# Performance work log

Hardware: AMD Instinct MI355X
Metric: run time of the kernel (lower is better)

## Reference

```python
import jax, jax.numpy as jnp
import numpy as np

D_MODEL = 1024
D_STATE = 16
D_CONV = 4
EXPAND = 2
D_INNER = EXPAND * D_MODEL
DT_RANK = (D_MODEL + 15) // 16  # ceil(d_model/16) = 64
BATCH = 2
SEQLEN = 1024


def _causal_conv_silu(x, w, b):
    # x: (B, d_inner, L); w: (d_inner, 1, k) depthwise; causal left padding k-1
    k = w.shape[-1]
    y = jax.lax.conv_general_dilated(
        x, w, window_strides=(1,), padding=[(k - 1, 0)],
        dimension_numbers=("NCH", "OIH", "NCH"), feature_group_count=x.shape[1])
    return jax.nn.silu(y + b[None, :, None])


def _ssm_scan(dA, dBx):
    # h_t = dA_t * h_{t-1} + dBx_t, parallel associative scan over L (axis=2)
    def op(e1, e2):
        a1, b1 = e1
        a2, b2 = e2
        return (a1 * a2, a2 * b1 + b2)
    return jax.lax.associative_scan(op, (dA, dBx), axis=2)[1]


def _mamba_dir(xz, conv_w, conv_b, xproj_w, dtproj_w, dt_bias, A_log, Dp):
    d_inner = xz.shape[1] // 2
    x, z = xz[:, :d_inner], xz[:, d_inner:]
    u = _causal_conv_silu(x, conv_w, conv_b)                  # (B, d, L)
    x_dbl = jnp.einsum('bdl,kd->bkl', u, xproj_w)             # (B, dt_rank+2n, L)
    n = A_log.shape[1]
    r = dtproj_w.shape[1]
    delta = jnp.einsum('dr,brl->bdl', dtproj_w, x_dbl[:, :r])
    Bm = x_dbl[:, r:r + n]                                    # (B, n, L)
    Cm = x_dbl[:, r + n:]                                     # (B, n, L)
    delta = jax.nn.softplus(delta + dt_bias[None, :, None])
    A = -jnp.exp(A_log)                                       # (d, n)
    dA = jnp.exp(jnp.einsum('bdl,dn->bdln', delta, A))
    dBx = jnp.einsum('bdl,bnl,bdl->bdln', delta, Bm, u)
    h = _ssm_scan(dA, dBx)                                    # (B, d, L, n)
    y = jnp.einsum('bdln,bnl->bdl', h, Cm)
    y = y + Dp[None, :, None] * u
    return y * jax.nn.silu(z)


def setup_inputs() -> dict:
    key = jax.random.key(0)
    ks = jax.random.split(key, 16)
    s_in = 1.0 / np.sqrt(D_MODEL)
    s_x = 1.0 / np.sqrt(D_INNER)
    dt_std = DT_RANK ** -0.5

    def dt_bias_init(k):
        dt = jnp.exp(jax.random.uniform(k, (D_INNER,)) * (np.log(0.1) - np.log(0.001)) + np.log(0.001))
        dt = jnp.clip(dt, 1e-4, None)
        return dt + jnp.log(-jnp.expm1(-dt))  # inverse softplus

    A_log = jnp.log(jnp.tile(jnp.arange(1, D_STATE + 1, dtype=jnp.float32)[None, :], (D_INNER, 1)))
    inp = {
        'hidden_states': jax.random.normal(ks[0], (BATCH, SEQLEN, D_MODEL), jnp.float32),
        'in_proj_w': jax.random.normal(ks[1], (2 * D_INNER, D_MODEL), jnp.float32) * s_in,
        'conv_w': jax.random.normal(ks[2], (D_INNER, 1, D_CONV), jnp.float32) * 0.3,
        'conv_bias': jnp.zeros((D_INNER,), jnp.float32),
        'x_proj_w': jax.random.normal(ks[3], (DT_RANK + 2 * D_STATE, D_INNER), jnp.float32) * s_x,
        'dt_proj_w': jax.random.uniform(ks[4], (D_INNER, DT_RANK), jnp.float32, -dt_std, dt_std),
        'dt_proj_bias': dt_bias_init(ks[5]),
        'A_log': A_log,
        'D_skip': jnp.ones((D_INNER,), jnp.float32),
        'convb_w': jax.random.normal(ks[6], (D_INNER, 1, D_CONV), jnp.float32) * 0.3,
        'convb_bias': jnp.zeros((D_INNER,), jnp.float32),
        'x_proj_b_w': jax.random.normal(ks[7], (DT_RANK + 2 * D_STATE, D_INNER), jnp.float32) * s_x,
        'dt_proj_b_w': jax.random.uniform(ks[8], (D_INNER, DT_RANK), jnp.float32, -dt_std, dt_std),
        'dt_proj_b_bias': dt_bias_init(ks[9]),
        'A_b_log': A_log,
        'D_b_skip': jnp.ones((D_INNER,), jnp.float32),
        'out_proj_w': jax.random.normal(ks[10], (D_MODEL, D_INNER), jnp.float32) * s_x,
    }
    return inp


def reference(hidden_states, in_proj_w, conv_w, conv_bias, x_proj_w, dt_proj_w,
              dt_proj_bias, A_log, D_skip, convb_w, convb_bias, x_proj_b_w,
              dt_proj_b_w, dt_proj_b_bias, A_b_log, D_b_skip, out_proj_w):
    # in_proj (no bias): (B, 2*d_inner, L)
    xz = jnp.einsum('ed,bld->bel', in_proj_w, hidden_states)
    out_f = _mamba_dir(xz, conv_w, conv_bias, x_proj_w, dt_proj_w, dt_proj_bias, A_log, D_skip)
    out_b = _mamba_dir(xz[:, :, ::-1], convb_w, convb_bias, x_proj_b_w, dt_proj_b_w,
                       dt_proj_b_bias, A_b_log, D_b_skip)[:, :, ::-1]
    # if_divide_out=False: just sum then out_proj (no bias)
    return jnp.einsum('bdl,od->blo', out_f + out_b, out_proj_w)
```

## Files before the change

kernel.cpp:

```cpp
#include <hip/hip_runtime.h>
#include <math.h>


typedef _Float16 f16x8 __attribute__((ext_vector_type(8)));
typedef _Float16 f16x4 __attribute__((ext_vector_type(4)));
typedef float    f32x4 __attribute__((ext_vector_type(4)));

#define SCH 32
#define SCL 32

__device__ __forceinline__ void gload_lds16(const void* g, void* l) {
    __builtin_amdgcn_global_load_lds(
        (const __attribute__((address_space(1))) void*)g,
        (__attribute__((address_space(3))) void*)l, 16, 0, 0);
}

__device__ __forceinline__ float softplus_f(float x) {
    float e = __builtin_amdgcn_exp2f(-fabsf(x) * 1.44269504f);
    return fmaxf(x, 0.f) + __builtin_amdgcn_logf(1.f + e) * 0.69314718f;
}

template<int CTRL>
__device__ __forceinline__ float dpp_add(float x) {
    int s = __builtin_amdgcn_update_dpp(0, __builtin_bit_cast(int, x),
                                        CTRL, 0xF, 0xF, true);
    return x + __builtin_bit_cast(float, s);
}

template<int WMW, int WNW, int FM, int FN>
__global__ __launch_bounds__(256)
void gemm_nt_f16(const _Float16* __restrict__ A, const _Float16* __restrict__ B,
                 float* __restrict__ C, int K, int ldc, long sA, long sC)
{
    constexpr int BM = WMW * FM * 16, BN = WNW * FN * 16;
    constexpr int ACH = BM / 8, NCH = (BM + BN) / 8;
    __shared__ __align__(16) _Float16 lds[(BM + BN) * 64];
    A += (long)blockIdx.z * sA;
    C += (long)blockIdx.z * sC;
    const int m0 = blockIdx.y * BM, n0 = blockIdx.x * BN;
    const int t = threadIdx.x, wid = t >> 6, lane = t & 63;
    const int wm = wid / WNW, wn = wid % WNW;
    const int srow = lane >> 3;
    const int skk  = ((lane & 7) ^ srow) * 8;

    f32x4 acc[FM][FN];
#pragma unroll
    for (int i = 0; i < FM; ++i)
#pragma unroll
        for (int j = 0; j < FN; ++j) acc[i][j] = (f32x4){0.f, 0.f, 0.f, 0.f};

    for (int k0 = 0; k0 < K; k0 += 64) {
#pragma unroll
        for (int c = wid; c < NCH; c += 4) {
            const _Float16* gp = (c < ACH)
                ? A + (long)(m0 + c * 8 + srow) * K + k0 + skk
                : B + (long)(n0 + (c - ACH) * 8 + srow) * K + k0 + skk;
            gload_lds16(gp, lds + c * 512);
        }
        __syncthreads();
#pragma unroll
        for (int kw = 0; kw < 2; ++kw) {
            f16x8 af[FM], bf[FN];
#pragma unroll
            for (int i = 0; i < FM; ++i) {
                int r = wm * FM * 16 + i * 16 + (lane & 15);
                af[i] = *(const f16x8*)(lds + r * 64 +
                        (((kw * 4 + (lane >> 4)) ^ (r & 7)) * 8));
            }
#pragma unroll
            for (int j = 0; j < FN; ++j) {
                int r = wn * FN * 16 + j * 16 + (lane & 15);
                bf[j] = *(const f16x8*)(lds + BM * 64 + r * 64 +
                        (((kw * 4 + (lane >> 4)) ^ (r & 7)) * 8));
            }
#pragma unroll
            for (int i = 0; i < FM; ++i)
#pragma unroll
                for (int j = 0; j < FN; ++j)
                    acc[i][j] = __builtin_amdgcn_mfma_f32_16x16x32_f16(
                        af[i], bf[j], acc[i][j], 0, 0, 0);
        }
        __syncthreads();
    }
#pragma unroll
    for (int i = 0; i < FM; ++i)
#pragma unroll
        for (int j = 0; j < FN; ++j) {
            int n = n0 + wn * FN * 16 + j * 16 + (lane & 15);
            int m = m0 + wm * FM * 16 + i * 16 + (lane >> 4) * 4;
            *(f32x4*)&C[(long)n * ldc + m] = acc[i][j];
        }
}

#define XP_SK 8
__global__ __launch_bounds__(256)
void xproj_f16_kernel(const float* __restrict__ u, const _Float16* __restrict__ xw16,
                      float* __restrict__ pb)
{
    __shared__ __align__(16) _Float16 Asw[128 * 64];
    __shared__ __align__(16) _Float16 Bsw[96 * 64];
    const int t = threadIdx.x, wid = t >> 6, lane = t & 63;
    const int wm = wid >> 1, wn = wid & 1;
    const int m0 = blockIdx.x * 128;
    const int sk = blockIdx.y, dirb = blockIdx.z;
    const float* ub = u + (long)dirb * 2048 * 1024;
    const _Float16* Bw = xw16 + (long)(dirb >> 1) * 96 * 2048;
    const int srow = lane >> 3;
    const int skk  = ((lane & 7) ^ srow) * 8;
    const int lloc = (t & 31) * 4;
    const int kslt = t >> 5;

    f32x4 acc[4][3];
#pragma unroll
    for (int i = 0; i < 4; ++i)
#pragma unroll
        for (int j = 0; j < 3; ++j) acc[i][j] = (f32x4){0.f, 0.f, 0.f, 0.f};

    for (int ks = 0; ks < 2048 / XP_SK; ks += 64) {
        const int k0 = sk * (2048 / XP_SK) + ks;
#pragma unroll
        for (int c = wid; c < 12; c += 4)
            gload_lds16(Bw + (long)(c * 8 + srow) * 2048 + k0 + skk, Bsw + c * 512);
        float av[8][4];
#pragma unroll
        for (int kk = 0; kk < 8; ++kk) {
            f32x4 v = *(const f32x4*)&ub[(long)(k0 + kslt * 8 + kk) * 1024 + m0 + lloc];
            av[kk][0] = v.x; av[kk][1] = v.y; av[kk][2] = v.z; av[kk][3] = v.w;
        }
#pragma unroll
        for (int q = 0; q < 4; ++q) {
            int l = lloc + q;
            f16x8 h = {(_Float16)av[0][q], (_Float16)av[1][q], (_Float16)av[2][q],
                       (_Float16)av[3][q], (_Float16)av[4][q], (_Float16)av[5][q],
                       (_Float16)av[6][q], (_Float16)av[7][q]};
            *(f16x8*)(Asw + l * 64 + ((kslt ^ (l & 7)) * 8)) = h;
        }
        __syncthreads();
#pragma unroll
        for (int kw = 0; kw < 2; ++kw) {
            f16x8 af[4], bf[3];
#pragma unroll
            for (int i = 0; i < 4; ++i) {
                int r = wm * 64 + i * 16 + (lane & 15);
                af[i] = *(const f16x8*)(Asw + r * 64 +
                        (((kw * 4 + (lane >> 4)) ^ (r & 7)) * 8));
            }
#pragma unroll
            for (int j = 0; j < 3; ++j) {
                int r = wn * 48 + j * 16 + (lane & 15);
                bf[j] = *(const f16x8*)(Bsw + r * 64 +
                        (((kw * 4 + (lane >> 4)) ^ (r & 7)) * 8));
            }
#pragma unroll
            for (int i = 0; i < 4; ++i)
#pragma unroll
                for (int j = 0; j < 3; ++j)
                    acc[i][j] = __builtin_amdgcn_mfma_f32_16x16x32_f16(
                        af[i], bf[j], acc[i][j], 0, 0, 0);
        }
        __syncthreads();
    }
    float* Cp = pb + ((long)sk * 4 + dirb) * 96 * 1024;
#pragma unroll
    for (int i = 0; i < 4; ++i)
#pragma unroll
        for (int j = 0; j < 3; ++j) {
            int n = wn * 48 + j * 16 + (lane & 15);
            int m = m0 + wm * 64 + i * 16 + (lane >> 4) * 4;
            *(f32x4*)&Cp[(long)n * 1024 + m] = acc[i][j];
        }
}

__global__ __launch_bounds__(256)
void xreduce_kernel(const float* __restrict__ pb, float* __restrict__ xdbl)
{
    int f = (blockIdx.x * 256 + threadIdx.x) * 4;
    f32x4 s = (f32x4){0.f, 0.f, 0.f, 0.f};
#pragma unroll
    for (int sk = 0; sk < XP_SK; ++sk)
        s += *(const f32x4*)(pb + (long)sk * 393216 + f);
    *(f32x4*)(xdbl + f) = s;
}

__global__ __launch_bounds__(256)
void dtproj_f16_kernel(const float* __restrict__ xdbl, const _Float16* __restrict__ dw16,
                       const float* __restrict__ bcat, float* __restrict__ delta)
{
    __shared__ __align__(16) _Float16 Asw[128 * 64];
    __shared__ __align__(16) _Float16 Bsw[128 * 64];
    const int t = threadIdx.x, wid = t >> 6, lane = t & 63;
    const int wm = wid >> 1, wn = wid & 1;
    const int n0 = blockIdx.x * 128, m0 = blockIdx.y * 128;
    const int dirb = blockIdx.z, dir = dirb >> 1;
    const float* Xb = xdbl + (long)dirb * 96 * 1024;
    const _Float16* Bw = dw16 + (long)dir * 2048 * 64;
    const int srow = lane >> 3, skk = ((lane & 7) ^ srow) * 8;
    const int lloc = (t & 31) * 4, kslt = t >> 5;

#pragma unroll
    for (int c = wid; c < 16; c += 4)
        gload_lds16(Bw + (long)(n0 + c * 8 + srow) * 64 + skk, Bsw + c * 512);
    float av[8][4];
#pragma unroll
    for (int kk = 0; kk < 8; ++kk) {
        f32x4 v = *(const f32x4*)&Xb[(long)(kslt * 8 + kk) * 1024 + m0 + lloc];
        av[kk][0] = v.x; av[kk][1] = v.y; av[kk][2] = v.z; av[kk][3] = v.w;
    }
#pragma unroll
    for (int q = 0; q < 4; ++q) {
        int l = lloc + q;
        f16x8 h = {(_Float16)av[0][q], (_Float16)av[1][q], (_Float16)av[2][q],
                   (_Float16)av[3][q], (_Float16)av[4][q], (_Float16)av[5][q],
                   (_Float16)av[6][q], (_Float16)av[7][q]};
        *(f16x8*)(Asw + l * 64 + ((kslt ^ (l & 7)) * 8)) = h;
    }
    __syncthreads();

    f32x4 acc[4][4];
#pragma unroll
    for (int i = 0; i < 4; ++i)
#pragma unroll
        for (int j = 0; j < 4; ++j) acc[i][j] = (f32x4){0.f, 0.f, 0.f, 0.f};
#pragma unroll
    for (int kw = 0; kw < 2; ++kw) {
        f16x8 af[4], bf[4];
#pragma unroll
        for (int i = 0; i < 4; ++i) {
            int r = wm * 64 + i * 16 + (lane & 15);
            af[i] = *(const f16x8*)(Asw + r * 64 +
                    (((kw * 4 + (lane >> 4)) ^ (r & 7)) * 8));
        }
#pragma unroll
        for (int j = 0; j < 4; ++j) {
            int r = wn * 64 + j * 16 + (lane & 15);
            bf[j] = *(const f16x8*)(Bsw + r * 64 +
                    (((kw * 4 + (lane >> 4)) ^ (r & 7)) * 8));
        }
#pragma unroll
        for (int i = 0; i < 4; ++i)
#pragma unroll
            for (int j = 0; j < 4; ++j)
                acc[i][j] = __builtin_amdgcn_mfma_f32_16x16x32_f16(
                    af[i], bf[j], acc[i][j], 0, 0, 0);
    }
    float* Dp = delta + (long)dirb * 2048 * 1024;
#pragma unroll
    for (int j = 0; j < 4; ++j) {
        int dd = n0 + wn * 64 + j * 16 + (lane & 15);
        float bm = bcat[dir * 2048 + dd];
#pragma unroll
        for (int i = 0; i < 4; ++i) {
            int m = m0 + wm * 64 + i * 16 + (lane >> 4) * 4;
            f32x4 v = acc[i][j];
            f32x4 o = {softplus_f(v.x + bm), softplus_f(v.y + bm),
                       softplus_f(v.z + bm), softplus_f(v.w + bm)};
            *(f32x4*)&Dp[(long)dd * 1024 + m] = o;
        }
    }
}

__global__ __launch_bounds__(256)
void cvt_f16_kernel(const float* __restrict__ in, _Float16* __restrict__ out, int n)
{
    int i = (blockIdx.x * 256 + threadIdx.x) * 4;
    if (i + 3 < n) {
        float4 v = *(const float4*)(in + i);
        f16x4 h = {(_Float16)v.x, (_Float16)v.y, (_Float16)v.z, (_Float16)v.w};
        *(f16x4*)(out + i) = h;
    }
}

__global__ __launch_bounds__(256)
void concat_weights(const float* __restrict__ xwf, const float* __restrict__ xwb,
                    const float* __restrict__ dwf, const float* __restrict__ dwb,
                    const float* __restrict__ bf,  const float* __restrict__ bb,
                    _Float16* __restrict__ xw16, _Float16* __restrict__ dw16,
                    float* __restrict__ bcat)
{
    int i = blockIdx.x * 256 + threadIdx.x;
    if (i < 196608) { xw16[i] = (_Float16)xwf[i]; xw16[196608 + i] = (_Float16)xwb[i]; }
    if (i < 131072) { dw16[i] = (_Float16)dwf[i]; dw16[131072 + i] = (_Float16)dwb[i]; }
    if (i < 2048)   { bcat[i]  = bf[i];  bcat[2048 + i] = bb[i]; }
}

__global__ __launch_bounds__(256)
void conv_silu_kernel(const float* __restrict__ xz,
                      const float* __restrict__ wf, const float* __restrict__ bf,
                      const float* __restrict__ wb, const float* __restrict__ bbk,
                      float* __restrict__ u)
{
    long idx = (long)blockIdx.x * 256 + threadIdx.x;
    int l = (int)(idx & 1023);
    long r = idx >> 10;
    int d = (int)(r & 2047);
    int b = (int)((r >> 11) & 1);
    int dir = (int)(r >> 12);
    const float* x = xz + ((long)b * 4096 + d) * 1024;
    const float* w = dir ? wb : wf;
    float s = dir ? bbk[d] : bf[d];
    if (dir == 0) {
#pragma unroll
        for (int j = 0; j < 4; ++j) {
            int p = l - 3 + j;
            if (p >= 0) s = fmaf(w[d * 4 + j], x[p], s);
        }
    } else {
#pragma unroll
        for (int j = 0; j < 4; ++j) {
            int src = l - 3 + j;
            if (src >= 0) s = fmaf(w[d * 4 + j], x[1023 - src], s);
        }
    }
    u[idx] = s / (1.f + __builtin_amdgcn_exp2f(-s * 1.44269504f));
}

__global__ __launch_bounds__(256)
void scan_p1_kernel(const float* __restrict__ u, const float* __restrict__ delta,
                    const float* __restrict__ xdbl,
                    const float* __restrict__ Alf, const float* __restrict__ Alb,
                    float* __restrict__ hend, float* __restrict__ aprod)
{
    __shared__ float sD[64][36], sU[64][36], sB[32][20];
    const int t = threadIdx.x, wid = t >> 6, lane = t & 63;
    const int nl = lane & 3;
    const int dloc = wid * 16 + (lane >> 2);
    const int dblk = blockIdx.x, chunk = blockIdx.y, dirb = blockIdx.z;
    const int d = dblk * 64 + dloc, dir = dirb >> 1;
    const int T0 = chunk * SCL;
    f32x4 Av = *(const f32x4*)((dir ? Alb : Alf) + d * 16 + nl * 4);
    float An2[4] = {-expf(Av.x) * 1.44269504f, -expf(Av.y) * 1.44269504f,
                    -expf(Av.z) * 1.44269504f, -expf(Av.w) * 1.44269504f};
    const float* dp = delta + ((long)dirb * 2048 + dblk * 64) * 1024;
    const float* up = u     + ((long)dirb * 2048 + dblk * 64) * 1024;
    const float* Bp = xdbl  + ((long)dirb * 96 + 64) * 1024;

#pragma unroll
    for (int rep = 0; rep < 2; ++rep) {
        int ii = rep * 256 + t;
        int dd = ii >> 3, q = ii & 7;
        *(f32x4*)&sD[dd][q * 4] = *(const f32x4*)&dp[(long)dd * 1024 + T0 + q * 4];
        *(f32x4*)&sU[dd][q * 4] = *(const f32x4*)&up[(long)dd * 1024 + T0 + q * 4];
    }
#pragma unroll
    for (int rep = 0; rep < 2; ++rep) {
        int ii = rep * 256 + t;
        int n = ii >> 5, tt = ii & 31;
        sB[tt][n] = Bp[(long)n * 1024 + T0 + tt];
    }
    __syncthreads();

    float h[4] = {0.f, 0.f, 0.f, 0.f};
    float S = 0.f;
#pragma unroll 4
    for (int g = 0; g < 8; ++g) {
        f32x4 dlv = *(const f32x4*)&sD[dloc][g * 4];
        f32x4 uuv = *(const f32x4*)&sU[dloc][g * 4];
        float dls[4] = {dlv.x, dlv.y, dlv.z, dlv.w};
        float uus[4] = {uuv.x, uuv.y, uuv.z, uuv.w};
#pragma unroll
        for (int r4 = 0; r4 < 4; ++r4) {
            f32x4 Bv = *(const f32x4*)&sB[g * 4 + r4][nl * 4];
            float Bs[4] = {Bv.x, Bv.y, Bv.z, Bv.w};
            float dl = dls[r4], t1 = dl * uus[r4];
            S += dl;
#pragma unroll
            for (int r = 0; r < 4; ++r)
                h[r] = fmaf(__builtin_amdgcn_exp2f(dl * An2[r]), h[r], t1 * Bs[r]);
        }
    }
    long cb = (((long)dirb * SCH + chunk) * 2048 + d) * 16 + nl * 4;
    *(f32x4*)&hend[cb]  = (f32x4){h[0], h[1], h[2], h[3]};
    *(f32x4*)&aprod[cb] = (f32x4){__builtin_amdgcn_exp2f(S * An2[0]),
                                  __builtin_amdgcn_exp2f(S * An2[1]),
                                  __builtin_amdgcn_exp2f(S * An2[2]),
                                  __builtin_amdgcn_exp2f(S * An2[3])};
}

__global__ __launch_bounds__(256)
void scan_carry_kernel(const float* __restrict__ hend, const float* __restrict__ aprod,
                       float* __restrict__ hinit)
{
    int f = blockIdx.x * 256 + threadIdx.x;
    int dn = f & 32767;
    int dirb = f >> 15;
    long src = (long)dirb * SCH * 32768 + dn;
    long dst = (long)(dirb >> 1) * 4194304 + (long)(dirb & 1) * 1048576 + dn;
    float hcur = 0.f;
#pragma unroll
    for (int c = 0; c < SCH; ++c) {
        hinit[dst + (long)c * 32768] = hcur;
        hcur = hend[src + (long)c * 32768]
             + aprod[src + (long)c * 32768] * hcur;
    }
}

__global__ __launch_bounds__(256)
void scan_p3_kernel(const float* __restrict__ u, const float* __restrict__ delta,
                    const float* __restrict__ xdbl,
                    const float* __restrict__ Alf, const float* __restrict__ Alb,
                    const float* __restrict__ Df, const float* __restrict__ Db,
                    const float* __restrict__ hinit, float* __restrict__ y)
{
    __shared__ float sD[64][36], sU[64][36], sB[32][20], sC[32][20];
    const int t = threadIdx.x, wid = t >> 6, lane = t & 63;
    const int nl = lane & 3;
    const int dloc = wid * 16 + (lane >> 2);
    const int dblk = blockIdx.x, chunk = blockIdx.y, dirb = blockIdx.z;
    const int d = dblk * 64 + dloc, dir = dirb >> 1;
    const int T0 = chunk * SCL;
    f32x4 Av = *(const f32x4*)((dir ? Alb : Alf) + d * 16 + nl * 4);
    float An2[4] = {-expf(Av.x) * 1.44269504f, -expf(Av.y) * 1.44269504f,
                    -expf(Av.z) * 1.44269504f, -expf(Av.w) * 1.44269504f};
    const float Dd = (dir ? Db : Df)[d];
    const float* dp = delta + ((long)dirb * 2048 + dblk * 64) * 1024;
    const float* up = u     + ((long)dirb * 2048 + dblk * 64) * 1024;
    const float* Bp = xdbl  + ((long)dirb * 96 + 64) * 1024;
    const float* Cp = xdbl  + ((long)dirb * 96 + 80) * 1024;
    float* yrow = y + ((long)dirb * 2048 + d) * 1024;

#pragma unroll
    for (int rep = 0; rep < 2; ++rep) {
        int ii = rep * 256 + t;
        int dd = ii >> 3, q = ii & 7;
        *(f32x4*)&sD[dd][q * 4] = *(const f32x4*)&dp[(long)dd * 1024 + T0 + q * 4];
        *(f32x4*)&sU[dd][q * 4] = *(const f32x4*)&up[(long)dd * 1024 + T0 + q * 4];
    }
#pragma unroll
    for (int rep = 0; rep < 2; ++rep) {
        int ii = rep * 256 + t;
        int n = ii >> 5, tt = ii & 31;
        sB[tt][n] = Bp[(long)n * 1024 + T0 + tt];
        sC[tt][n] = Cp[(long)n * 1024 + T0 + tt];
    }
    long cb = (long)(dirb >> 1) * 4194304 + (long)(dirb & 1) * 1048576
            + (long)chunk * 32768 + (long)d * 16 + nl * 4;
    f32x4 h0v = *(const f32x4*)&hinit[cb];
    float h[4] = {h0v.x, h0v.y, h0v.z, h0v.w};
    const bool m[4] = {nl == 0, nl == 1, nl == 2, nl == 3};
    __syncthreads();

#pragma unroll 4
    for (int g = 0; g < 8; ++g) {
        f32x4 dlv = *(const f32x4*)&sD[dloc][g * 4];
        f32x4 uuv = *(const f32x4*)&sU[dloc][g * 4];
        float dls[4] = {dlv.x, dlv.y, dlv.z, dlv.w};
        float uus[4] = {uuv.x, uuv.y, uuv.z, uuv.w};
        float keep = 0.f;
#pragma unroll
        for (int r4 = 0; r4 < 4; ++r4) {
            f32x4 Bv = *(const f32x4*)&sB[g * 4 + r4][nl * 4];
            f32x4 Cv = *(const f32x4*)&sC[g * 4 + r4][nl * 4];
            float Bs[4] = {Bv.x, Bv.y, Bv.z, Bv.w};
            float Cs[4] = {Cv.x, Cv.y, Cv.z, Cv.w};
            float dl = dls[r4], uu = uus[r4];
            float t1 = dl * uu;
#pragma unroll
            for (int r = 0; r < 4; ++r)
                h[r] = fmaf(__builtin_amdgcn_exp2f(dl * An2[r]), h[r], t1 * Bs[r]);
            float p = h[0] * Cs[0];
            p = fmaf(h[1], Cs[1], p);
            p = fmaf(h[2], Cs[2], p);
            p = fmaf(h[3], Cs[3], p);
            p = dpp_add<0xB1>(p);
            p = dpp_add<0x4E>(p);
            float fy = fmaf(Dd, uu, p);
            keep = m[r4] ? fy : keep;
        }
        yrow[T0 + g * 4 + nl] = keep;
    }
}

__global__ __launch_bounds__(256)
void combine_T_kernel(const float* __restrict__ xz, const float* __restrict__ y,
                      _Float16* __restrict__ GT)
{
    __shared__ float Ls[64][65];
    const int d0 = blockIdx.x * 64, l0 = blockIdx.y * 64, b = blockIdx.z;
    const int t = threadIdx.x;
#pragma unroll
    for (int rep = 0; rep < 4; ++rep) {
        int i = rep * 256 + t;
        int dl = i >> 4;
        int lq = (i & 15) * 4;
        const float* zp  = xz + ((long)b * 4096 + 2048 + d0 + dl) * 1024 + l0 + lq;
        const float* yfp = y  + ((long)(b)     * 2048 + d0 + dl) * 1024 + l0 + lq;
        const float* ybp = y  + ((long)(2 + b) * 2048 + d0 + dl) * 1024 + (1020 - l0 - lq);
        float4 vz = *(const float4*)zp;
        float4 vf = *(const float4*)yfp;
        float4 vb = *(const float4*)ybp;
        float zz[4]  = {vz.x, vz.y, vz.z, vz.w};
        float ff[4]  = {vf.x, vf.y, vf.z, vf.w};
        float bbv[4] = {vb.w, vb.z, vb.y, vb.x};
#pragma unroll
        for (int qq = 0; qq < 4; ++qq) {
            float z = zz[qq];
            float sz = z / (1.f + __builtin_amdgcn_exp2f(-z * 1.44269504f));
            Ls[dl][lq + qq] = sz * (ff[qq] + bbv[qq]);
        }
    }
    __syncthreads();
#pragma unroll
    for (int rep = 0; rep < 4; ++rep) {
        int i = rep * 256 + t;
        int ll = i >> 4;
        int dq = (i & 15) * 4;
        f16x4 h = {(_Float16)Ls[dq][ll], (_Float16)Ls[dq + 1][ll],
                   (_Float16)Ls[dq + 2][ll], (_Float16)Ls[dq + 3][ll]};
        *(f16x4*)(GT + ((long)(b * 1024 + l0 + ll)) * 2048 + d0 + dq) = h;
    }
}

extern "C" void kernel_launch(void* const* d_in, const int* in_sizes, int n_in,
                              void* d_out, int out_size, void* d_ws, size_t ws_size,
                              hipStream_t stream)
{
    const float* hidden   = (const float*)d_in[0];
    const float* inproj_w = (const float*)d_in[1];
    const float* conv_w   = (const float*)d_in[2];
    const float* conv_b   = (const float*)d_in[3];
    const float* xproj_w  = (const float*)d_in[4];
    const float* dtproj_w = (const float*)d_in[5];
    const float* dt_bias  = (const float*)d_in[6];
    const float* A_log    = (const float*)d_in[7];
    const float* D_skip   = (const float*)d_in[8];
    const float* convb_w  = (const float*)d_in[9];
    const float* convb_b  = (const float*)d_in[10];
    const float* xprojb_w = (const float*)d_in[11];
    const float* dtprojb_w= (const float*)d_in[12];
    const float* dtb_bias = (const float*)d_in[13];
    const float* Ab_log   = (const float*)d_in[14];
    const float* Db_skip  = (const float*)d_in[15];
    const float* outproj_w= (const float*)d_in[16];
    float* out = (float*)d_out;

    float* ws    = (float*)d_ws;
    float* xz    = ws;
    float* u     = ws + 8388608;
    float* xdbl  = ws + 16777216;
    float* delta = ws + 17170432;
    float* y     = ws + 25559040;
    _Float16* H16    = (_Float16*)u;
    _Float16* Win16  = (_Float16*)(u + 1048576);
    float*    xpb    = delta;
    _Float16* GT     = (_Float16*)delta;
    _Float16* Wout16 = (_Float16*)y;
    _Float16* dw16   = (_Float16*)y;
    float*    bcat   = y + 131072;
    _Float16* xw16   = (_Float16*)(y + 135168);
    float* hend  = y;
    float* aprod = y + 4194304;
    float* hinit = xz;

    hipLaunchKernelGGL(cvt_f16_kernel, dim3(2048), dim3(256), 0, stream,
        hidden, H16, 2097152);
    hipLaunchKernelGGL(cvt_f16_kernel, dim3(4096), dim3(256), 0, stream,
        inproj_w, Win16, 4194304);

    hipLaunchKernelGGL(concat_weights, dim3(768), dim3(256), 0, stream,
        xproj_w, xprojb_w, dtproj_w, dtprojb_w, dt_bias, dtb_bias,
        xw16, dw16, bcat);

    hipLaunchKernelGGL((gemm_nt_f16<2, 2, 4, 4>),
        dim3(32, 8, 2), dim3(256), 0, stream,
        H16, Win16, xz, 1024, 1024, 1048576L, 4194304L);

    hipLaunchKernelGGL(conv_silu_kernel, dim3(32768), dim3(256), 0, stream,
        xz, conv_w, conv_b, convb_w, convb_b, u);

    hipLaunchKernelGGL(xproj_f16_kernel, dim3(8, XP_SK, 4), dim3(256), 0, stream,
        u, xw16, xpb);
    hipLaunchKernelGGL(xreduce_kernel, dim3(384), dim3(256), 0, stream,
        xpb, xdbl);

    hipLaunchKernelGGL(dtproj_f16_kernel, dim3(16, 8, 4), dim3(256), 0, stream,
        xdbl, dw16, bcat, delta);

    hipLaunchKernelGGL(scan_p1_kernel, dim3(32, SCH, 4), dim3(256), 0, stream,
        u, delta, xdbl, A_log, Ab_log, hend, aprod);
    hipLaunchKernelGGL(scan_carry_kernel, dim3(512), dim3(256), 0, stream,
        hend, aprod, hinit);
    hipLaunchKernelGGL(scan_p3_kernel, dim3(32, SCH, 4), dim3(256), 0, stream,
        u, delta, xdbl, A_log, Ab_log, D_skip, Db_skip, hinit, y);

    hipLaunchKernelGGL(combine_T_kernel, dim3(32, 16, 2), dim3(256), 0, stream,
        xz, y, GT);

    hipLaunchKernelGGL(cvt_f16_kernel, dim3(2048), dim3(256), 0, stream,
        outproj_w, Wout16, 2097152);

    hipLaunchKernelGGL((gemm_nt_f16<4, 1, 2, 4>),
        dim3(32, 8, 1), dim3(256), 0, stream,
        Wout16, GT, out, 2048, 1024, 0L, 0L);
}
```

Measured before the change: 199.8 us.

## Store u, delta and y intermediates in fp16 and merge setup conversions

The conv/silu output u, the softplus delta and the scan output y are now kept as fp16 instead of fp32, halving the traffic of the memory-bound scan passes, the x-projection and the combine kernel. The separate weight and input conversion launches, including the out-proj weight conversion, are folded into one setup kernel. Workspace offsets are rearranged to fit the new fp16 buffers. Precision drops for delta and u in the recurrence, which may raise numerical error.

```diff
diff --git a/kernel.cpp b/kernel.cpp
--- a/kernel.cpp
+++ b/kernel.cpp
@@ -94,7 +94,7 @@
 
 #define XP_SK 8
 __global__ __launch_bounds__(256)
-void xproj_f16_kernel(const float* __restrict__ u, const _Float16* __restrict__ xw16,
+void xproj_f16_kernel(const _Float16* __restrict__ u16, const _Float16* __restrict__ xw16,
                       float* __restrict__ pb)
 {
     __shared__ __align__(16) _Float16 Asw[128 * 64];
@@ -103,7 +103,7 @@
     const int wm = wid >> 1, wn = wid & 1;
     const int m0 = blockIdx.x * 128;
     const int sk = blockIdx.y, dirb = blockIdx.z;
-    const float* ub = u + (long)dirb * 2048 * 1024;
+    const _Float16* ub = u16 + (long)dirb * 2048 * 1024;
     const _Float16* Bw = xw16 + (long)(dirb >> 1) * 96 * 2048;
     const int srow = lane >> 3;
     const int skk  = ((lane & 7) ^ srow) * 8;
@@ -121,18 +121,17 @@
 #pragma unroll
         for (int c = wid; c < 12; c += 4)
             gload_lds16(Bw + (long)(c * 8 + srow) * 2048 + k0 + skk, Bsw + c * 512);
-        float av[8][4];
+        _Float16 av[8][4];
 #pragma unroll
         for (int kk = 0; kk < 8; ++kk) {
-            f32x4 v = *(const f32x4*)&ub[(long)(k0 + kslt * 8 + kk) * 1024 + m0 + lloc];
-            av[kk][0] = v.x; av[kk][1] = v.y; av[kk][2] = v.z; av[kk][3] = v.w;
+            f16x4 v = *(const f16x4*)&ub[(long)(k0 + kslt * 8 + kk) * 1024 + m0 + lloc];
+            av[kk][0] = v[0]; av[kk][1] = v[1]; av[kk][2] = v[2]; av[kk][3] = v[3];
         }
 #pragma unroll
         for (int q = 0; q < 4; ++q) {
             int l = lloc + q;
-            f16x8 h = {(_Float16)av[0][q], (_Float16)av[1][q], (_Float16)av[2][q],
-                       (_Float16)av[3][q], (_Float16)av[4][q], (_Float16)av[5][q],
-                       (_Float16)av[6][q], (_Float16)av[7][q]};
+            f16x8 h = {av[0][q], av[1][q], av[2][q], av[3][q],
+                       av[4][q], av[5][q], av[6][q], av[7][q]};
             *(f16x8*)(Asw + l * 64 + ((kslt ^ (l & 7)) * 8)) = h;
         }
         __syncthreads();
@@ -184,7 +183,7 @@
 
 __global__ __launch_bounds__(256)
 void dtproj_f16_kernel(const float* __restrict__ xdbl, const _Float16* __restrict__ dw16,
-                       const float* __restrict__ bcat, float* __restrict__ delta)
+                       const float* __restrict__ bcat, _Float16* __restrict__ delta16)
 {
     __shared__ __align__(16) _Float16 Asw[128 * 64];
     __shared__ __align__(16) _Float16 Bsw[128 * 64];
@@ -243,7 +242,7 @@
                 acc[i][j] = __builtin_amdgcn_mfma_f32_16x16x32_f16(
                     af[i], bf[j], acc[i][j], 0, 0, 0);
     }
-    float* Dp = delta + (long)dirb * 2048 * 1024;
+    _Float16* Dp = delta16 + (long)dirb * 2048 * 1024;
 #pragma unroll
     for (int j = 0; j < 4; ++j) {
         int dd = n0 + wn * 64 + j * 16 + (lane & 15);
@@ -252,42 +251,53 @@
         for (int i = 0; i < 4; ++i) {
             int m = m0 + wm * 64 + i * 16 + (lane >> 4) * 4;
             f32x4 v = acc[i][j];
-            f32x4 o = {softplus_f(v.x + bm), softplus_f(v.y + bm),
-                       softplus_f(v.z + bm), softplus_f(v.w + bm)};
-            *(f32x4*)&Dp[(long)dd * 1024 + m] = o;
-        }
-    }
-}
-
-__global__ __launch_bounds__(256)
-void cvt_f16_kernel(const float* __restrict__ in, _Float16* __restrict__ out, int n)
-{
-    int i = (blockIdx.x * 256 + threadIdx.x) * 4;
-    if (i + 3 < n) {
-        float4 v = *(const float4*)(in + i);
-        f16x4 h = {(_Float16)v.x, (_Float16)v.y, (_Float16)v.z, (_Float16)v.w};
-        *(f16x4*)(out + i) = h;
-    }
-}
-
-__global__ __launch_bounds__(256)
-void concat_weights(const float* __restrict__ xwf, const float* __restrict__ xwb,
-                    const float* __restrict__ dwf, const float* __restrict__ dwb,
-                    const float* __restrict__ bf,  const float* __restrict__ bb,
-                    _Float16* __restrict__ xw16, _Float16* __restrict__ dw16,
-                    float* __restrict__ bcat)
-{
-    int i = blockIdx.x * 256 + threadIdx.x;
-    if (i < 196608) { xw16[i] = (_Float16)xwf[i]; xw16[196608 + i] = (_Float16)xwb[i]; }
-    if (i < 131072) { dw16[i] = (_Float16)dwf[i]; dw16[131072 + i] = (_Float16)dwb[i]; }
-    if (i < 2048)   { bcat[i]  = bf[i];  bcat[2048 + i] = bb[i]; }
+            f16x4 o = {(_Float16)softplus_f(v.x + bm), (_Float16)softplus_f(v.y + bm),
+                       (_Float16)softplus_f(v.z + bm), (_Float16)softplus_f(v.w + bm)};
+            *(f16x4*)&Dp[(long)dd * 1024 + m] = o;
+        }
+    }
+}
+
+__global__ __launch_bounds__(256)
+void setup_kernel(const float* __restrict__ hidden, const float* __restrict__ winp,
+                  const float* __restrict__ woutp,
+                  const float* __restrict__ xwf, const float* __restrict__ xwb,
+                  const float* __restrict__ dwf, const float* __restrict__ dwb,
+                  const float* __restrict__ bf,  const float* __restrict__ bb,
+                  _Float16* __restrict__ H16, _Float16* __restrict__ Win16,
+                  _Float16* __restrict__ Wout16,
+                  _Float16* __restrict__ xw16, _Float16* __restrict__ dw16,
+                  float* __restrict__ bcat)
+{
+    long i4 = ((long)blockIdx.x * 256 + threadIdx.x) * 4;
+    auto cvt4 = [](const float* s) -> f16x4 {
+        float4 v = *(const float4*)s;
+        return (f16x4){(_Float16)v.x, (_Float16)v.y, (_Float16)v.z, (_Float16)v.w};
+    };
+    if (i4 < 4194304) *(f16x4*)(Win16 + i4) = cvt4(winp + i4);
+    if (i4 < 2097152) {
+        *(f16x4*)(H16 + i4)   = cvt4(hidden + i4);
+        *(f16x4*)(Wout16 + i4) = cvt4(woutp + i4);
+    }
+    if (i4 < 196608) {
+        *(f16x4*)(xw16 + i4)          = cvt4(xwf + i4);
+        *(f16x4*)(xw16 + 196608 + i4) = cvt4(xwb + i4);
+    }
+    if (i4 < 131072) {
+        *(f16x4*)(dw16 + i4)          = cvt4(dwf + i4);
+        *(f16x4*)(dw16 + 131072 + i4) = cvt4(dwb + i4);
+    }
+    if (i4 < 2048) {
+        *(float4*)(bcat + i4)        = *(const float4*)(bf + i4);
+        *(float4*)(bcat + 2048 + i4) = *(const float4*)(bb + i4);
+    }
 }
 
 __global__ __launch_bounds__(256)
 void conv_silu_kernel(const float* __restrict__ xz,
                       const float* __restrict__ wf, const float* __restrict__ bf,
                       const float* __restrict__ wb, const float* __restrict__ bbk,
-                      float* __restrict__ u)
+                      _Float16* __restrict__ u16)
 {
     long idx = (long)blockIdx.x * 256 + threadIdx.x;
     int l = (int)(idx & 1023);
@@ -311,16 +321,17 @@
             if (src >= 0) s = fmaf(w[d * 4 + j], x[1023 - src], s);
         }
     }
-    u[idx] = s / (1.f + __builtin_amdgcn_exp2f(-s * 1.44269504f));
-}
-
-__global__ __launch_bounds__(256)
-void scan_p1_kernel(const float* __restrict__ u, const float* __restrict__ delta,
+    u16[idx] = (_Float16)(s / (1.f + __builtin_amdgcn_exp2f(-s * 1.44269504f)));
+}
+
+__global__ __launch_bounds__(256)
+void scan_p1_kernel(const _Float16* __restrict__ u16, const _Float16* __restrict__ delta16,
                     const float* __restrict__ xdbl,
                     const float* __restrict__ Alf, const float* __restrict__ Alb,
                     float* __restrict__ hend, float* __restrict__ aprod)
 {
-    __shared__ float sD[64][36], sU[64][36], sB[32][20];
+    __shared__ _Float16 sD[64][40], sU[64][40];
+    __shared__ float sB[32][20];
     const int t = threadIdx.x, wid = t >> 6, lane = t & 63;
     const int nl = lane & 3;
     const int dloc = wid * 16 + (lane >> 2);
@@ -330,16 +341,14 @@
     f32x4 Av = *(const f32x4*)((dir ? Alb : Alf) + d * 16 + nl * 4);
     float An2[4] = {-expf(Av.x) * 1.44269504f, -expf(Av.y) * 1.44269504f,
                     -expf(Av.z) * 1.44269504f, -expf(Av.w) * 1.44269504f};
-    const float* dp = delta + ((long)dirb * 2048 + dblk * 64) * 1024;
-    const float* up = u     + ((long)dirb * 2048 + dblk * 64) * 1024;
-    const float* Bp = xdbl  + ((long)dirb * 96 + 64) * 1024;
-
-#pragma unroll
-    for (int rep = 0; rep < 2; ++rep) {
-        int ii = rep * 256 + t;
-        int dd = ii >> 3, q = ii & 7;
-        *(f32x4*)&sD[dd][q * 4] = *(const f32x4*)&dp[(long)dd * 1024 + T0 + q * 4];
-        *(f32x4*)&sU[dd][q * 4] = *(const f32x4*)&up[(long)dd * 1024 + T0 + q * 4];
+    const _Float16* dp = delta16 + ((long)dirb * 2048 + dblk * 64) * 1024;
+    const _Float16* up = u16    + ((long)dirb * 2048 + dblk * 64) * 1024;
+    const float* Bp = xdbl + ((long)dirb * 96 + 64) * 1024;
+
+    {
+        int dd = t >> 2, q = t & 3;
+        *(f16x8*)&sD[dd][q * 8] = *(const f16x8*)&dp[(long)dd * 1024 + T0 + q * 8];
+        *(f16x8*)&sU[dd][q * 8] = *(const f16x8*)&up[(long)dd * 1024 + T0 + q * 8];
     }
 #pragma unroll
     for (int rep = 0; rep < 2; ++rep) {
@@ -353,10 +362,10 @@
     float S = 0.f;
 #pragma unroll 4
     for (int g = 0; g < 8; ++g) {
-        f32x4 dlv = *(const f32x4*)&sD[dloc][g * 4];
-        f32x4 uuv = *(const f32x4*)&sU[dloc][g * 4];
-        float dls[4] = {dlv.x, dlv.y, dlv.z, dlv.w};
-        float uus[4] = {uuv.x, uuv.y, uuv.z, uuv.w};
+        f16x4 dlh = *(const f16x4*)&sD[dloc][g * 4];
+        f16x4 uuh = *(const f16x4*)&sU[dloc][g * 4];
+        float dls[4] = {(float)dlh[0], (float)dlh[1], (float)dlh[2], (float)dlh[3]};
+        float uus[4] = {(float)uuh[0], (float)uuh[1], (float)uuh[2], (float)uuh[3]};
 #pragma unroll
         for (int r4 = 0; r4 < 4; ++r4) {
             f32x4 Bv = *(const f32x4*)&sB[g * 4 + r4][nl * 4];
@@ -395,13 +404,14 @@
 }
 
 __global__ __launch_bounds__(256)
-void scan_p3_kernel(const float* __restrict__ u, const float* __restrict__ delta,
+void scan_p3_kernel(const _Float16* __restrict__ u16, const _Float16* __restrict__ delta16,
                     const float* __restrict__ xdbl,
                     const float* __restrict__ Alf, const float* __restrict__ Alb,
                     const float* __restrict__ Df, const float* __restrict__ Db,
-                    const float* __restrict__ hinit, float* __restrict__ y)
-{
-    __shared__ float sD[64][36], sU[64][36], sB[32][20], sC[32][20];
+                    const float* __restrict__ hinit, _Float16* __restrict__ y16)
+{
+    __shared__ _Float16 sD[64][40], sU[64][40];
+    __shared__ float sB[32][20], sC[32][20];
     const int t = threadIdx.x, wid = t >> 6, lane = t & 63;
     const int nl = lane & 3;
     const int dloc = wid * 16 + (lane >> 2);
@@ -412,18 +422,16 @@
     float An2[4] = {-expf(Av.x) * 1.44269504f, -expf(Av.y) * 1.44269504f,
                     -expf(Av.z) * 1.44269504f, -expf(Av.w) * 1.44269504f};
     const float Dd = (dir ? Db : Df)[d];
-    const float* dp = delta + ((long)dirb * 2048 + dblk * 64) * 1024;
-    const float* up = u     + ((long)dirb * 2048 + dblk * 64) * 1024;
-    const float* Bp = xdbl  + ((long)dirb * 96 + 64) * 1024;
-    const float* Cp = xdbl  + ((long)dirb * 96 + 80) * 1024;
-    float* yrow = y + ((long)dirb * 2048 + d) * 1024;
-
-#pragma unroll
-    for (int rep = 0; rep < 2; ++rep) {
-        int ii = rep * 256 + t;
-        int dd = ii >> 3, q = ii & 7;
-        *(f32x4*)&sD[dd][q * 4] = *(const f32x4*)&dp[(long)dd * 1024 + T0 + q * 4];
-        *(f32x4*)&sU[dd][q * 4] = *(const f32x4*)&up[(long)dd * 1024 + T0 + q * 4];
+    const _Float16* dp = delta16 + ((long)dirb * 2048 + dblk * 64) * 1024;
+    const _Float16* up = u16    + ((long)dirb * 2048 + dblk * 64) * 1024;
+    const float* Bp = xdbl + ((long)dirb * 96 + 64) * 1024;
+    const float* Cp = xdbl + ((long)dirb * 96 + 80) * 1024;
+    _Float16* yrow = y16 + ((long)dirb * 2048 + d) * 1024;
+
+    {
+        int dd = t >> 2, q = t & 3;
+        *(f16x8*)&sD[dd][q * 8] = *(const f16x8*)&dp[(long)dd * 1024 + T0 + q * 8];
+        *(f16x8*)&sU[dd][q * 8] = *(const f16x8*)&up[(long)dd * 1024 + T0 + q * 8];
     }
 #pragma unroll
     for (int rep = 0; rep < 2; ++rep) {
@@ -441,10 +449,10 @@
 
 #pragma unroll 4
     for (int g = 0; g < 8; ++g) {
-        f32x4 dlv = *(const f32x4*)&sD[dloc][g * 4];
-        f32x4 uuv = *(const f32x4*)&sU[dloc][g * 4];
-        float dls[4] = {dlv.x, dlv.y, dlv.z, dlv.w};
-        float uus[4] = {uuv.x, uuv.y, uuv.z, uuv.w};
+        f16x4 dlh = *(const f16x4*)&sD[dloc][g * 4];
+        f16x4 uuh = *(const f16x4*)&sU[dloc][g * 4];
+        float dls[4] = {(float)dlh[0], (float)dlh[1], (float)dlh[2], (float)dlh[3]};
+        float uus[4] = {(float)uuh[0], (float)uuh[1], (float)uuh[2], (float)uuh[3]};
         float keep = 0.f;
 #pragma unroll
         for (int r4 = 0; r4 < 4; ++r4) {
@@ -466,12 +474,12 @@
             float fy = fmaf(Dd, uu, p);
             keep = m[r4] ? fy : keep;
         }
-        yrow[T0 + g * 4 + nl] = keep;
-    }
-}
-
-__global__ __launch_bounds__(256)
-void combine_T_kernel(const float* __restrict__ xz, const float* __restrict__ y,
+        yrow[T0 + g * 4 + nl] = (_Float16)keep;
+    }
+}
+
+__global__ __launch_bounds__(256)
+void combine_T_kernel(const float* __restrict__ xz, const _Float16* __restrict__ y16,
                       _Float16* __restrict__ GT)
 {
     __shared__ float Ls[64][65];
@@ -482,15 +490,15 @@
         int i = rep * 256 + t;
         int dl = i >> 4;
         int lq = (i & 15) * 4;
-        const float* zp  = xz + ((long)b * 4096 + 2048 + d0 + dl) * 1024 + l0 + lq;
-        const float* yfp = y  + ((long)(b)     * 2048 + d0 + dl) * 1024 + l0 + lq;
-        const float* ybp = y  + ((long)(2 + b) * 2048 + d0 + dl) * 1024 + (1020 - l0 - lq);
+        const float* zp = xz + ((long)b * 4096 + 2048 + d0 + dl) * 1024 + l0 + lq;
+        const _Float16* yfp = y16 + ((long)(b)     * 2048 + d0 + dl) * 1024 + l0 + lq;
+        const _Float16* ybp = y16 + ((long)(2 + b) * 2048 + d0 + dl) * 1024 + (1020 - l0 - lq);
         float4 vz = *(const float4*)zp;
-        float4 vf = *(const float4*)yfp;
-        float4 vb = *(const float4*)ybp;
+        f16x4 vf = *(const f16x4*)yfp;
+        f16x4 vb = *(const f16x4*)ybp;
         float zz[4]  = {vz.x, vz.y, vz.z, vz.w};
-        float ff[4]  = {vf.x, vf.y, vf.z, vf.w};
-        float bbv[4] = {vb.w, vb.z, vb.y, vb.x};
+        float ff[4]  = {(float)vf[0], (float)vf[1], (float)vf[2], (float)vf[3]};
+        float bbv[4] = {(float)vb[3], (float)vb[2], (float)vb[1], (float)vb[0]};
 #pragma unroll
         for (int qq = 0; qq < 4; ++qq) {
             float z = zz[qq];
@@ -541,52 +549,47 @@
     float* y     = ws + 25559040;
     _Float16* H16    = (_Float16*)u;
     _Float16* Win16  = (_Float16*)(u + 1048576);
-    float*    xpb    = delta;
-    _Float16* GT     = (_Float16*)delta;
-    _Float16* Wout16 = (_Float16*)y;
-    _Float16* dw16   = (_Float16*)y;
-    float*    bcat   = y + 131072;
-    _Float16* xw16   = (_Float16*)(y + 135168);
+    _Float16* u16    = (_Float16*)(u + 3145728);
+    _Float16* Wout16 = (_Float16*)(u + 7340032);
+    _Float16* delta16 = (_Float16*)delta;
+    float*    xpb     = delta + 4194304;
+    _Float16* GT      = (_Float16*)delta;
+    _Float16* dw16  = (_Float16*)y;
+    float*    bcat  = y + 131072;
+    _Float16* xw16  = (_Float16*)(y + 135168);
     float* hend  = y;
     float* aprod = y + 4194304;
+    _Float16* y16 = (_Float16*)y;
     float* hinit = xz;
 
-    hipLaunchKernelGGL(cvt_f16_kernel, dim3(2048), dim3(256), 0, stream,
-        hidden, H16, 2097152);
-    hipLaunchKernelGGL(cvt_f16_kernel, dim3(4096), dim3(256), 0, stream,
-        inproj_w, Win16, 4194304);
-
-    hipLaunchKernelGGL(concat_weights, dim3(768), dim3(256), 0, stream,
-        xproj_w, xprojb_w, dtproj_w, dtprojb_w, dt_bias, dtb_bias,
-        xw16, dw16, bcat);
+    hipLaunchKernelGGL(setup_kernel, dim3(4096), dim3(256), 0, stream,
+        hidden, inproj_w, outproj_w, xproj_w, xprojb_w, dtproj_w, dtprojb_w,
+        dt_bias, dtb_bias, H16, Win16, Wout16, xw16, dw16, bcat);
 
     hipLaunchKernelGGL((gemm_nt_f16<2, 2, 4, 4>),
         dim3(32, 8, 2), dim3(256), 0, stream,
         H16, Win16, xz, 1024, 1024, 1048576L, 4194304L);
 
     hipLaunchKernelGGL(conv_silu_kernel, dim3(32768), dim3(256), 0, stream,
-        xz, conv_w, conv_b, convb_w, convb_b, u);
+        xz, conv_w, conv_b, convb_w, convb_b, u16);
 
     hipLaunchKernelGGL(xproj_f16_kernel, dim3(8, XP_SK, 4), dim3(256), 0, stream,
-        u, xw16, xpb);
+        u16, xw16, xpb);
     hipLaunchKernelGGL(xreduce_kernel, dim3(384), dim3(256), 0, stream,
         xpb, xdbl);
 
     hipLaunchKernelGGL(dtproj_f16_kernel, dim3(16, 8, 4), dim3(256), 0, stream,
-        xdbl, dw16, bcat, delta);
+        xdbl, dw16, bcat, delta16);
 
     hipLaunchKernelGGL(scan_p1_kernel, dim3(32, SCH, 4), dim3(256), 0, stream,
-        u, delta, xdbl, A_log, Ab_log, hend, aprod);
+        u16, delta16, xdbl, A_log, Ab_log, hend, aprod);
     hipLaunchKernelGGL(scan_carry_kernel, dim3(512), dim3(256), 0, stream,
         hend, aprod, hinit);
     hipLaunchKernelGGL(scan_p3_kernel, dim3(32, SCH, 4), dim3(256), 0, stream,
-        u, delta, xdbl, A_log, Ab_log, D_skip, Db_skip, hinit, y);
+        u16, delta16, xdbl, A_log, Ab_log, D_skip, Db_skip, hinit, y16);
 
     hipLaunchKernelGGL(combine_T_kernel, dim3(32, 16, 2), dim3(256), 0, stream,
-        xz, y, GT);
-
-    hipLaunchKernelGGL(cvt_f16_kernel, dim3(2048), dim3(256), 0, stream,
-        outproj_w, Wout16, 2097152);
+        xz, y16, GT);
 
     hipLaunchKernelGGL((gemm_nt_f16<4, 1, 2, 4>),
         dim3(32, 8, 1), dim3(256), 0, stream,
```

New measurement: 180.8 us. 9.5% less time.
